# Optimization experiments

Hardware: AMD Instinct MI355X
Metric: run time of the kernel (lower is better)

## Reference

```python
import jax, jax.numpy as jnp
import numpy as np

T = 8192      # num tokens
D = 2048      # model_dim
E = 64        # num_experts
RED = 4       # xmoe reduced dim
CAP = 2 * ((T + E - 1) // E)  # 256, capacity = 2*ceil(T/E)


def setup_inputs() -> dict:
    key = jax.random.key(0)
    k1, k2, k3 = jax.random.split(key, 3)
    x = jax.random.normal(k1, (T, D), dtype=jnp.float32)
    w_red = jax.random.normal(k2, (RED, D), dtype=jnp.float32) * 0.02   # dim_reduction weight [4, D]
    centroids = jax.random.normal(k3, (E, RED), dtype=jnp.float32) * 0.32  # expert_centroids [E, 4]
    return {"x": x, "w_red": w_red, "centroids": centroids}


def reference(x, w_red, centroids):
    eps_norm = 1e-4
    f32 = jnp.float32
    # xmoe path: dim reduction then cosine logits
    h = x @ w_red.T                                        # [T, 4]
    c = centroids * (1.5 / jnp.linalg.norm(centroids, axis=1, keepdims=True))  # in-place renorm to 1.5
    cn = c / jnp.maximum(jnp.linalg.norm(c, axis=1, keepdims=True), eps_norm)  # F.normalize(eps=1e-4)
    logits = h @ cn.T                                      # [T, E]
    # _make_finite
    ok = jnp.isfinite(logits)
    min_fin = jnp.min(jnp.where(ok, logits, jnp.inf))
    logits = jnp.where(ok, logits, min_fin)

    gates = jax.nn.softmax(logits, axis=1)                 # [T, E]
    idx1 = jnp.argmax(gates, axis=1)                       # [T]
    mask1 = jax.nn.one_hot(idx1, E, dtype=jnp.int32)       # [T, E]
    # second expert: argmax of logits with top-1 masked out (policy 'none' -> no noise)
    logits_except1 = jnp.where(mask1.astype(bool), -jnp.inf, logits)
    idx2 = jnp.argmax(logits_except1, axis=1)
    mask2 = jax.nn.one_hot(idx2, E, dtype=jnp.int32)

    # metadata: per-expert token counts (== sort/unique_consecutive result)
    splits1 = mask1.sum(axis=0)                            # [E]
    splits2 = mask2.sum(axis=0)

    # positions within each expert's buffer
    loc1 = jnp.cumsum(mask1, axis=0) - 1                   # [T, E]
    loc2 = jnp.cumsum(mask2, axis=0) - 1 + mask1.sum(axis=0, keepdims=True)

    # load-balancing aux loss (before capacity drop)
    me = gates.mean(axis=0)
    ce = mask1.astype(gates.dtype).mean(axis=0)
    l_aux = jnp.mean(me * ce) * E * E

    # drop tokens over capacity
    mask1 = mask1 * (loc1 < CAP).astype(mask1.dtype)
    mask2 = mask2 * (loc2 < CAP).astype(mask2.dtype)

    # gate probs, normalized after dropping (normalize_gate_prob_before_dropping=False)
    g1 = (gates * mask1).sum(axis=1)
    g2 = (gates * mask2).sum(axis=1)
    denom = jnp.maximum(g1 + g2, jnp.finfo(gates.dtype).eps)
    g1 = g1 / denom
    g2 = g2 / denom

    loc1_s = (loc1 * mask1).sum(axis=1)                    # [T]
    loc2_s = (loc2 * mask2).sum(axis=1)
    oh1 = jax.nn.one_hot(loc1_s, CAP, dtype=f32)           # [T, CAP]
    oh2 = jax.nn.one_hot(loc2_s, CAP, dtype=f32)

    # combine_weights[t, e, c] = g_s[t] * mask[t, e] * onehot_cap[t, c]
    combine = ((g1[:, None] * mask1.astype(f32))[:, :, None] * oh1[:, None, :]
               + (g2[:, None] * mask2.astype(f32))[:, :, None] * oh2[:, None, :])  # [T, E, CAP]
    dispatch = combine > 0
    return (l_aux, combine, dispatch, splits1, splits2)
```

## Files before the change

### kernel.cpp

```cpp
#include <hip/hip_runtime.h>
#include <hip/hip_bf16.h>
#include <math.h>

#define T_TOK 8192
#define DIM   2048
#define NEXP  64
#define RED   4
#define CAP   256
#define NBLK_GATE (T_TOK/4)

__global__ __launch_bounds__(256) void gate_kernel(
    const float* __restrict__ x, const float* __restrict__ w_red,
    const float* __restrict__ centroids,
    int* __restrict__ idx1, int* __restrict__ idx2,
    float* __restrict__ g1raw, float* __restrict__ g2raw,
    float* __restrict__ me_acc)
{
    __shared__ float4 s_w[RED * (DIM/4)];
    __shared__ float  s_cn[NEXP][RED];
    __shared__ float  s_gate[4][NEXP];

    const int tid  = threadIdx.x;
    const int lane = tid & 63;
    const int wave = tid >> 6;

    const float4* w4 = (const float4*)w_red;
    for (int i = tid; i < RED * (DIM/4); i += 256) s_w[i] = w4[i];

    if (tid < NEXP) {
        float c0 = centroids[tid*RED+0], c1 = centroids[tid*RED+1];
        float c2 = centroids[tid*RED+2], c3 = centroids[tid*RED+3];
        float n  = sqrtf(c0*c0 + c1*c1 + c2*c2 + c3*c3);
        float sc = 1.5f / n;
        float d0 = c0*sc, d1 = c1*sc, d2 = c2*sc, d3 = c3*sc;
        float n2 = sqrtf(d0*d0 + d1*d1 + d2*d2 + d3*d3);
        float inv = 1.0f / fmaxf(n2, 1e-4f);
        s_cn[tid][0] = d0*inv; s_cn[tid][1] = d1*inv;
        s_cn[tid][2] = d2*inv; s_cn[tid][3] = d3*inv;
    }
    __syncthreads();

    const int t = blockIdx.x * 4 + wave;
    const float4* x4 = (const float4*)(x + (size_t)t * DIM);

    float h0 = 0.f, h1 = 0.f, h2 = 0.f, h3 = 0.f;
#pragma unroll
    for (int i = 0; i < (DIM/4)/64; ++i) {
        int j = lane + i * 64;
        float4 xv = x4[j];
        float4 w0 = s_w[0*(DIM/4) + j];
        float4 w1 = s_w[1*(DIM/4) + j];
        float4 w2 = s_w[2*(DIM/4) + j];
        float4 w3 = s_w[3*(DIM/4) + j];
        h0 += xv.x*w0.x + xv.y*w0.y + xv.z*w0.z + xv.w*w0.w;
        h1 += xv.x*w1.x + xv.y*w1.y + xv.z*w1.z + xv.w*w1.w;
        h2 += xv.x*w2.x + xv.y*w2.y + xv.z*w2.z + xv.w*w2.w;
        h3 += xv.x*w3.x + xv.y*w3.y + xv.z*w3.z + xv.w*w3.w;
    }
#pragma unroll
    for (int m = 32; m; m >>= 1) {
        h0 += __shfl_xor(h0, m); h1 += __shfl_xor(h1, m);
        h2 += __shfl_xor(h2, m); h3 += __shfl_xor(h3, m);
    }

    float logit = h0*s_cn[lane][0] + h1*s_cn[lane][1]
                + h2*s_cn[lane][2] + h3*s_cn[lane][3];

    float mx = logit;
#pragma unroll
    for (int m = 32; m; m >>= 1) mx = fmaxf(mx, __shfl_xor(mx, m));
    float p = __expf(logit - mx);
    float s = p;
#pragma unroll
    for (int m = 32; m; m >>= 1) s += __shfl_xor(s, m);

    float bv = logit; int bi = lane;
#pragma unroll
    for (int m = 32; m; m >>= 1) {
        float ov = __shfl_xor(bv, m); int oi = __shfl_xor(bi, m);
        if (ov > bv || (ov == bv && oi < bi)) { bv = ov; bi = oi; }
    }
    const int i1 = bi;

    float v2 = (lane == i1) ? -INFINITY : logit;
    float bv2 = v2; int bi2 = lane;
#pragma unroll
    for (int m = 32; m; m >>= 1) {
        float ov = __shfl_xor(bv2, m); int oi = __shfl_xor(bi2, m);
        if (ov > bv2 || (ov == bv2 && oi < bi2)) { bv2 = ov; bi2 = oi; }
    }
    const int i2 = bi2;

    float g1 = __shfl(p, i1) / s;
    float g2 = __shfl(p, i2) / s;

    if (lane == 0) {
        idx1[t] = i1; idx2[t] = i2;
        g1raw[t] = g1; g2raw[t] = g2;
    }

    s_gate[wave][lane] = p / s;
    __syncthreads();
    if (tid < NEXP) {
        float acc = s_gate[0][tid] + s_gate[1][tid] + s_gate[2][tid] + s_gate[3][tid];
        atomicAdd(&me_acc[tid], acc);
    }
}

__global__ __launch_bounds__(256) void count_kernel(
    const int* __restrict__ idx1, const int* __restrict__ idx2,
    int* __restrict__ pos1, int* __restrict__ pos2,
    int* __restrict__ splits1_i,
    float* __restrict__ out_splits1, float* __restrict__ out_splits2)
{
    const int e = blockIdx.x;
    const int tid = threadIdx.x, lane = tid & 63, wave = tid >> 6;
    __shared__ int wtot[4];

    int run = 0;
    for (int base = 0; base < T_TOK; base += 256) {
        int t = base + tid;
        bool m = (idx1[t] == e);
        unsigned long long b = __ballot(m);
        int rank = __popcll(b & ((1ull << lane) - 1ull));
        if (lane == 0) wtot[wave] = __popcll(b);
        __syncthreads();
        int pre = 0;
        for (int w = 0; w < wave; ++w) pre += wtot[w];
        int tot = wtot[0] + wtot[1] + wtot[2] + wtot[3];
        if (m) pos1[t] = run + pre + rank;
        run += tot;
        __syncthreads();
    }
    const int split1 = run;

    int run2 = 0;
    for (int base = 0; base < T_TOK; base += 256) {
        int t = base + tid;
        bool m = (idx2[t] == e);
        unsigned long long b = __ballot(m);
        int rank = __popcll(b & ((1ull << lane) - 1ull));
        if (lane == 0) wtot[wave] = __popcll(b);
        __syncthreads();
        int pre = 0;
        for (int w = 0; w < wave; ++w) pre += wtot[w];
        int tot = wtot[0] + wtot[1] + wtot[2] + wtot[3];
        if (m) pos2[t] = split1 + run2 + pre + rank;
        run2 += tot;
        __syncthreads();
    }

    if (tid == 0) {
        splits1_i[e] = split1;
        out_splits1[e] = (float)split1;
        out_splits2[e] = (float)run2;
    }
}

__global__ __launch_bounds__(64) void laux_kernel(
    const float* __restrict__ me_acc, const int* __restrict__ splits1_i,
    float* __restrict__ out0)
{
    const int tid = threadIdx.x;
    float me = me_acc[tid] / (float)T_TOK;
    float ce = (float)splits1_i[tid] / (float)T_TOK;
    float v = me * ce;
#pragma unroll
    for (int m = 32; m; m >>= 1) v += __shfl_xor(v, m);
    if (tid == 0) out0[0] = v * (float)NEXP;
}

__global__ __launch_bounds__(256) void scatter_kernel(
    const int* __restrict__ idx1, const int* __restrict__ idx2,
    const int* __restrict__ pos1, const int* __restrict__ pos2,
    const float* __restrict__ g1raw, const float* __restrict__ g2raw,
    float* __restrict__ combine, float* __restrict__ dispatch)
{
    int t = blockIdx.x * 256 + threadIdx.x;
    if (t >= T_TOK) return;
    int p1 = pos1[t], p2 = pos2[t];
    bool k1 = p1 < CAP, k2 = p2 < CAP;
    float g1 = k1 ? g1raw[t] : 0.f;
    float g2 = k2 ? g2raw[t] : 0.f;
    float denom = fmaxf(g1 + g2, 1.1920929e-07f);
    g1 /= denom; g2 /= denom;
    size_t base = (size_t)t * (NEXP * CAP);
    if (k1) {
        size_t o = base + (size_t)idx1[t] * CAP + p1;
        combine[o]  = g1;
        dispatch[o] = (g1 > 0.f) ? 1.f : 0.f;
    }
    if (k2) {
        size_t o = base + (size_t)idx2[t] * CAP + p2;
        combine[o]  = g2;
        dispatch[o] = (g2 > 0.f) ? 1.f : 0.f;
    }
}

extern "C" void kernel_launch(void* const* d_in, const int* in_sizes, int n_in,
                              void* d_out, int out_size, void* d_ws, size_t ws_size,
                              hipStream_t stream) {
    const float* x         = (const float*)d_in[0];
    const float* w_red     = (const float*)d_in[1];
    const float* centroids = (const float*)d_in[2];

    float* out = (float*)d_out;
    const size_t TEC = (size_t)T_TOK * NEXP * CAP;
    float* combine  = out + 1;
    float* dispatch = out + 1 + TEC;
    float* out_s1   = out + 1 + 2*TEC;
    float* out_s2   = out + 1 + 2*TEC + NEXP;

    int*   idx1     = (int*)d_ws;
    int*   idx2     = idx1 + T_TOK;
    int*   pos1     = idx2 + T_TOK;
    int*   pos2     = pos1 + T_TOK;
    float* g1raw    = (float*)(pos2 + T_TOK);
    float* g2raw    = g1raw + T_TOK;
    int*   splits1i = (int*)(g2raw + T_TOK);
    float* me_acc   = (float*)(splits1i + NEXP);

    hipMemsetAsync(me_acc, 0, NEXP * sizeof(float), stream);

    hipMemsetAsync(d_out, 0, (size_t)out_size * sizeof(float), stream);

    gate_kernel<<<NBLK_GATE, 256, 0, stream>>>(x, w_red, centroids,
                                               idx1, idx2, g1raw, g2raw, me_acc);

    count_kernel<<<NEXP, 256, 0, stream>>>(idx1, idx2, pos1, pos2,
                                           splits1i, out_s1, out_s2);

    laux_kernel<<<1, 64, 0, stream>>>(me_acc, splits1i, out);

    scatter_kernel<<<(T_TOK + 255)/256, 256, 0, stream>>>(idx1, idx2, pos1, pos2,
                                                          g1raw, g2raw, combine, dispatch);
}
```

Baseline: 1.136 ms.

## Replace memset with vectorized fill kernel and batch gate tokens per block

Replaces hipMemsetAsync of the large output with a grid-stride float4 zero-fill kernel. The gate kernel now processes 16 tokens per block so the shared copy of w_red is loaded fewer times. Per-block expert probability sums are written to a partial buffer instead of atomics, and laux reduces them. The cost is fewer gate blocks and a possibly less tuned fill than the runtime memset.

```diff
diff --git a/kernel.cpp b/kernel.cpp
--- a/kernel.cpp
+++ b/kernel.cpp
@@ -7,14 +7,26 @@
 #define NEXP  64
 #define RED   4
 #define CAP   256
-#define NBLK_GATE (T_TOK/4)
+#define TOK_PER_BLK 16
+#define NBLK_GATE (T_TOK/TOK_PER_BLK)
+
+__global__ __launch_bounds__(256) void fill_kernel(float* __restrict__ out, size_t n) {
+    size_t i = (size_t)blockIdx.x * blockDim.x + threadIdx.x;
+    size_t stride = (size_t)gridDim.x * blockDim.x;
+    size_t n4 = n >> 2;
+    float4 z = make_float4(0.f, 0.f, 0.f, 0.f);
+    float4* o4 = (float4*)out;
+    for (size_t j = i; j < n4; j += stride) o4[j] = z;
+    size_t tail = n - (n4 << 2);
+    if (i < tail) out[(n4 << 2) + i] = 0.f;
+}
 
 __global__ __launch_bounds__(256) void gate_kernel(
     const float* __restrict__ x, const float* __restrict__ w_red,
     const float* __restrict__ centroids,
     int* __restrict__ idx1, int* __restrict__ idx2,
     float* __restrict__ g1raw, float* __restrict__ g2raw,
-    float* __restrict__ me_acc)
+    float* __restrict__ mepart)
 {
     __shared__ float4 s_w[RED * (DIM/4)];
     __shared__ float  s_cn[NEXP][RED];
@@ -40,70 +52,76 @@
     }
     __syncthreads();
 
-    const int t = blockIdx.x * 4 + wave;
-    const float4* x4 = (const float4*)(x + (size_t)t * DIM);
-
-    float h0 = 0.f, h1 = 0.f, h2 = 0.f, h3 = 0.f;
-#pragma unroll
-    for (int i = 0; i < (DIM/4)/64; ++i) {
-        int j = lane + i * 64;
-        float4 xv = x4[j];
-        float4 w0 = s_w[0*(DIM/4) + j];
-        float4 w1 = s_w[1*(DIM/4) + j];
-        float4 w2 = s_w[2*(DIM/4) + j];
-        float4 w3 = s_w[3*(DIM/4) + j];
-        h0 += xv.x*w0.x + xv.y*w0.y + xv.z*w0.z + xv.w*w0.w;
-        h1 += xv.x*w1.x + xv.y*w1.y + xv.z*w1.z + xv.w*w1.w;
-        h2 += xv.x*w2.x + xv.y*w2.y + xv.z*w2.z + xv.w*w2.w;
-        h3 += xv.x*w3.x + xv.y*w3.y + xv.z*w3.z + xv.w*w3.w;
-    }
-#pragma unroll
-    for (int m = 32; m; m >>= 1) {
-        h0 += __shfl_xor(h0, m); h1 += __shfl_xor(h1, m);
-        h2 += __shfl_xor(h2, m); h3 += __shfl_xor(h3, m);
-    }
-
-    float logit = h0*s_cn[lane][0] + h1*s_cn[lane][1]
-                + h2*s_cn[lane][2] + h3*s_cn[lane][3];
-
-    float mx = logit;
-#pragma unroll
-    for (int m = 32; m; m >>= 1) mx = fmaxf(mx, __shfl_xor(mx, m));
-    float p = __expf(logit - mx);
-    float s = p;
-#pragma unroll
-    for (int m = 32; m; m >>= 1) s += __shfl_xor(s, m);
-
-    float bv = logit; int bi = lane;
-#pragma unroll
-    for (int m = 32; m; m >>= 1) {
-        float ov = __shfl_xor(bv, m); int oi = __shfl_xor(bi, m);
-        if (ov > bv || (ov == bv && oi < bi)) { bv = ov; bi = oi; }
-    }
-    const int i1 = bi;
-
-    float v2 = (lane == i1) ? -INFINITY : logit;
-    float bv2 = v2; int bi2 = lane;
-#pragma unroll
-    for (int m = 32; m; m >>= 1) {
-        float ov = __shfl_xor(bv2, m); int oi = __shfl_xor(bi2, m);
-        if (ov > bv2 || (ov == bv2 && oi < bi2)) { bv2 = ov; bi2 = oi; }
-    }
-    const int i2 = bi2;
-
-    float g1 = __shfl(p, i1) / s;
-    float g2 = __shfl(p, i2) / s;
-
-    if (lane == 0) {
-        idx1[t] = i1; idx2[t] = i2;
-        g1raw[t] = g1; g2raw[t] = g2;
-    }
-
-    s_gate[wave][lane] = p / s;
+    float me_local = 0.f;
+
+#pragma unroll
+    for (int it = 0; it < 4; ++it) {
+        const int t = blockIdx.x * TOK_PER_BLK + wave * 4 + it;
+        const float4* x4 = (const float4*)(x + (size_t)t * DIM);
+
+        float h0 = 0.f, h1 = 0.f, h2 = 0.f, h3 = 0.f;
+#pragma unroll
+        for (int i = 0; i < (DIM/4)/64; ++i) {
+            int j = lane + i * 64;
+            float4 xv = x4[j];
+            float4 w0 = s_w[0*(DIM/4) + j];
+            float4 w1 = s_w[1*(DIM/4) + j];
+            float4 w2 = s_w[2*(DIM/4) + j];
+            float4 w3 = s_w[3*(DIM/4) + j];
+            h0 += xv.x*w0.x + xv.y*w0.y + xv.z*w0.z + xv.w*w0.w;
+            h1 += xv.x*w1.x + xv.y*w1.y + xv.z*w1.z + xv.w*w1.w;
+            h2 += xv.x*w2.x + xv.y*w2.y + xv.z*w2.z + xv.w*w2.w;
+            h3 += xv.x*w3.x + xv.y*w3.y + xv.z*w3.z + xv.w*w3.w;
+        }
+#pragma unroll
+        for (int m = 32; m; m >>= 1) {
+            h0 += __shfl_xor(h0, m); h1 += __shfl_xor(h1, m);
+            h2 += __shfl_xor(h2, m); h3 += __shfl_xor(h3, m);
+        }
+
+        float logit = h0*s_cn[lane][0] + h1*s_cn[lane][1]
+                    + h2*s_cn[lane][2] + h3*s_cn[lane][3];
+
+        float mx = logit;
+#pragma unroll
+        for (int m = 32; m; m >>= 1) mx = fmaxf(mx, __shfl_xor(mx, m));
+        float p = __expf(logit - mx);
+        float s = p;
+#pragma unroll
+        for (int m = 32; m; m >>= 1) s += __shfl_xor(s, m);
+
+        float bv = logit; int bi = lane;
+#pragma unroll
+        for (int m = 32; m; m >>= 1) {
+            float ov = __shfl_xor(bv, m); int oi = __shfl_xor(bi, m);
+            if (ov > bv || (ov == bv && oi < bi)) { bv = ov; bi = oi; }
+        }
+        const int i1 = bi;
+
+        float v2 = (lane == i1) ? -INFINITY : logit;
+        float bv2 = v2; int bi2 = lane;
+#pragma unroll
+        for (int m = 32; m; m >>= 1) {
+            float ov = __shfl_xor(bv2, m); int oi = __shfl_xor(bi2, m);
+            if (ov > bv2 || (ov == bv2 && oi < bi2)) { bv2 = ov; bi2 = oi; }
+        }
+        const int i2 = bi2;
+
+        float g1 = __shfl(p, i1) / s;
+        float g2 = __shfl(p, i2) / s;
+
+        if (lane == 0) {
+            idx1[t] = i1; idx2[t] = i2;
+            g1raw[t] = g1; g2raw[t] = g2;
+        }
+        me_local += p / s;
+    }
+
+    s_gate[wave][lane] = me_local;
     __syncthreads();
     if (tid < NEXP) {
         float acc = s_gate[0][tid] + s_gate[1][tid] + s_gate[2][tid] + s_gate[3][tid];
-        atomicAdd(&me_acc[tid], acc);
+        mepart[(size_t)tid * NBLK_GATE + blockIdx.x] = acc;
     }
 }
 
@@ -157,17 +175,31 @@
     }
 }
 
-__global__ __launch_bounds__(64) void laux_kernel(
-    const float* __restrict__ me_acc, const int* __restrict__ splits1_i,
+__global__ __launch_bounds__(256) void laux_kernel(
+    const float* __restrict__ mepart, const int* __restrict__ splits1_i,
     float* __restrict__ out0)
 {
     const int tid = threadIdx.x;
-    float me = me_acc[tid] / (float)T_TOK;
-    float ce = (float)splits1_i[tid] / (float)T_TOK;
-    float v = me * ce;
-#pragma unroll
-    for (int m = 32; m; m >>= 1) v += __shfl_xor(v, m);
-    if (tid == 0) out0[0] = v * (float)NEXP;
+    const int e = tid >> 2, j = tid & 3;
+    const float* p = mepart + (size_t)e * NBLK_GATE + j * (NBLK_GATE/4);
+    float s = 0.f;
+    for (int i = 0; i < NBLK_GATE/4; ++i) s += p[i];
+    s += __shfl_xor(s, 1);
+    s += __shfl_xor(s, 2);
+
+    __shared__ float red[NEXP];
+    if (j == 0) {
+        float me = s / (float)T_TOK;
+        float ce = (float)splits1_i[e] / (float)T_TOK;
+        red[e] = me * ce;
+    }
+    __syncthreads();
+    if (tid < NEXP) {
+        float v = red[tid];
+#pragma unroll
+        for (int m = 32; m; m >>= 1) v += __shfl_xor(v, m);
+        if (tid == 0) out0[0] = v * (float)NEXP;
+    }
 }
 
 __global__ __launch_bounds__(256) void scatter_kernel(
@@ -218,19 +250,17 @@
     float* g1raw    = (float*)(pos2 + T_TOK);
     float* g2raw    = g1raw + T_TOK;
     int*   splits1i = (int*)(g2raw + T_TOK);
-    float* me_acc   = (float*)(splits1i + NEXP);
-
-    hipMemsetAsync(me_acc, 0, NEXP * sizeof(float), stream);
-
-    hipMemsetAsync(d_out, 0, (size_t)out_size * sizeof(float), stream);
+    float* mepart   = (float*)(splits1i + NEXP);
+
+    fill_kernel<<<2048, 256, 0, stream>>>(out, (size_t)out_size);
 
     gate_kernel<<<NBLK_GATE, 256, 0, stream>>>(x, w_red, centroids,
-                                               idx1, idx2, g1raw, g2raw, me_acc);
+                                               idx1, idx2, g1raw, g2raw, mepart);
 
     count_kernel<<<NEXP, 256, 0, stream>>>(idx1, idx2, pos1, pos2,
                                            splits1i, out_s1, out_s2);
 
-    laux_kernel<<<1, 64, 0, stream>>>(me_acc, splits1i, out);
+    laux_kernel<<<1, 256, 0, stream>>>(mepart, splits1i, out);
 
     scatter_kernel<<<(T_TOK + 255)/256, 256, 0, stream>>>(idx1, idx2, pos1, pos2,
                                                           g1raw, g2raw, combine, dispatch);
```

After: 1.183 ms. 1.04x slower.
